# Performance work log

Measured on AMD Instinct MI355X. Metric: run time of the kernel, lower is better.

The kernel has to match this reference:

```python
import jax, jax.numpy as jnp
import numpy as np


def segment_softmax(logits, seg, num_seg):
    m = jax.ops.segment_max(logits, seg, num_segments=num_seg)
    z = jnp.exp(logits - m[seg])
    s = jax.ops.segment_sum(z, seg, num_segments=num_seg)
    return z / s[seg]


def hconv(x_lin, edge_node, edge_he, num_nodes, num_edges, bias, alpha=None):
    # PyG HypergraphConv (heads=1, concat=True): D^-1 H W_e B^-1 H^T X Theta
    ones = jnp.ones(edge_node.shape[0], x_lin.dtype)
    D = jax.ops.segment_sum(ones, edge_node, num_segments=num_nodes)
    Dinv = jnp.where(D > 0, 1.0 / D, 0.0)
    Bd = jax.ops.segment_sum(ones, edge_he, num_segments=num_edges)
    Binv = jnp.where(Bd > 0, 1.0 / Bd, 0.0)
    # node -> hyperedge
    msg = Binv[edge_he][:, None] * x_lin[edge_node]
    if alpha is not None:
        msg = alpha[:, None] * msg
    e = jax.ops.segment_sum(msg, edge_he, num_segments=num_edges)
    # hyperedge -> node
    msg2 = Dinv[edge_node][:, None] * e[edge_he]
    if alpha is not None:
        msg2 = alpha[:, None] * msg2
    out = jax.ops.segment_sum(msg2, edge_node, num_segments=num_nodes)
    return out + bias


def reference(c_it, medicine_it, c_embeddings, m_embeddings, W_conv, b_conv, W_gat, att, b_gat, he_attr):
    nd = c_embeddings.shape[0]  # all indicators are 1 -> nonzero indexing is identity
    nm = m_embeddings.shape[0]
    oc = W_conv.shape[0]

    # diagnosis hypergraph: single hyperedge containing all diseases
    dia_x = c_embeddings @ W_conv.T  # [nd, oc]
    dia_nf = hconv(dia_x, jnp.arange(nd), jnp.zeros(nd, jnp.int32), nd, 1, b_conv)

    # medicine hypergraph: single hyperedge containing all medicines
    med_x = m_embeddings @ W_conv.T  # [nm, oc]
    med_nf = hconv(med_x, jnp.arange(nm), jnp.zeros(nm, jnp.int32), nm, 1, b_conv)

    # dia-med hypergraph: nd hyperedges, hyperedge d = {disease d} U {all medicines}
    comb = jnp.concatenate([c_embeddings, m_embeddings], axis=0)  # [nd+nm, in]
    x_lin = comb @ W_gat.T                                        # [nd+nm, oc]
    he_lin = he_attr @ W_gat.T                                    # [nd, oc]
    med_nodes = jnp.arange(nd, nd + nm)
    edge_node = jnp.concatenate(
        [jnp.arange(nd)[:, None], jnp.broadcast_to(med_nodes[None, :], (nd, nm))], axis=1
    ).reshape(-1)                              # [nd*(nm+1)]
    edge_he = jnp.repeat(jnp.arange(nd), nm + 1)

    # attention (attention_mode='node'): alpha from source node + hyperedge attr, softmax per hyperedge
    a_node = x_lin @ att[:oc]   # [nd+nm]
    a_he = he_lin @ att[oc:]    # [nd]
    logits = jax.nn.leaky_relu(a_node[edge_node] + a_he[edge_he], 0.2)
    alpha = segment_softmax(logits, edge_he, nd)

    dm_nf = hconv(x_lin, edge_node, edge_he, nd + nm, nd, b_gat, alpha)  # [nd+nm, oc]

    disease_final = jnp.concatenate([dm_nf[:nd], dia_nf], axis=1)   # [nd, 2*oc]
    medicine_final = jnp.concatenate([dm_nf[nd:], med_nf], axis=1)  # [nm, 2*oc]
    return jnp.concatenate([disease_final, medicine_final], axis=0)  # [nd+nm, 2*oc]


def setup_inputs() -> dict:
    key = jax.random.key(0)
    ks = jax.random.split(key, 8)
    ND, NM, IN, OUT = 2048, 512, 256, 128
    s = 0.05
    return {
        "c_it": jnp.ones((ND,), jnp.int32),
        "medicine_it": jnp.ones((NM,), jnp.int32),
        "c_embeddings": jax.random.normal(ks[0], (ND, IN), jnp.float32),
        "m_embeddings": jax.random.normal(ks[1], (NM, IN), jnp.float32),
        "W_conv": jax.random.normal(ks[2], (OUT, IN), jnp.float32) * s,
        "b_conv": jax.random.normal(ks[3], (OUT,), jnp.float32) * s,
        "W_gat": jax.random.normal(ks[4], (OUT, IN), jnp.float32) * s,
        "att": jax.random.normal(ks[5], (2 * OUT,), jnp.float32) * s,
        "b_gat": jax.random.normal(ks[6], (OUT,), jnp.float32) * s,
        "he_attr": jax.random.normal(ks[7], (ND, IN), jnp.float32),
    }
```

## Files before the change

kernel.cpp:

```cpp
#include <hip/hip_runtime.h>

#define ND 2048
#define NM 512
#define DIN 256
#define OC 128
#define NTOT (ND + NM)
#define NE (NM + 1)

#define WS_MEANC 0
#define WS_MEANM 256
#define WS_WE    512
#define WS_DIA   768
#define WS_MED   896
#define WS_AHE   1024
#define WS_ANODE 3072
#define WS_CD    5632
#define WS_XLIN  7680
#define WS_PART1 (WS_XLIN + NTOT * OC)
#define WS_PART2 (WS_PART1 + 84 * 256)

__device__ __forceinline__ float lrelu(float x) { return x > 0.f ? x : 0.2f * x; }

__global__ void kA1(const float* __restrict__ c_emb, const float* __restrict__ m_emb,
                    const float* __restrict__ W_gat, const float* __restrict__ att,
                    float* __restrict__ ws) {
    const int b = blockIdx.x;
    const int t = threadIdx.x;
    float acc = 0.f;
    if (b < 64) {
        const float* src = c_emb + (size_t)b * 32 * DIN;
        for (int r = 0; r < 32; ++r) acc += src[r * DIN + t];
    } else if (b < 80) {
        const float* src = m_emb + (size_t)(b - 64) * 32 * DIN;
        for (int r = 0; r < 32; ++r) acc += src[r * DIN + t];
    } else {
        const int o0 = (b - 80) * 32;
        for (int r = 0; r < 32; ++r)
            acc += W_gat[(size_t)(o0 + r) * DIN + t] * att[OC + o0 + r];
    }
    ws[WS_PART1 + b * 256 + t] = acc;
}

__global__ void kA2(float* __restrict__ ws) {
    const int t = threadIdx.x;
    const float* p = ws + WS_PART1;
    float sc = 0.f, sm = 0.f, sw = 0.f;
    for (int b = 0;  b < 64; ++b) sc += p[b * 256 + t];
    for (int b = 64; b < 80; ++b) sm += p[b * 256 + t];
    for (int b = 80; b < 84; ++b) sw += p[b * 256 + t];
    ws[WS_MEANC + t] = sc * (1.f / ND);
    ws[WS_MEANM + t] = sm * (1.f / NM);
    ws[WS_WE + t]    = sw;
}

__global__ void kB(const float* __restrict__ W_conv, const float* __restrict__ b_conv,
                   const float* __restrict__ he_attr, float* __restrict__ ws) {
    if (blockIdx.x == 0) {
        const int o = threadIdx.x;
        if (o < OC) {
            const float* mc = ws + WS_MEANC;
            const float* mm = ws + WS_MEANM;
            const float* wr = W_conv + (size_t)o * DIN;
            float a = 0.f, b = 0.f;
            for (int i = 0; i < DIN; ++i) {
                float w = wr[i];
                a = fmaf(mc[i], w, a);
                b = fmaf(mm[i], w, b);
            }
            float bc = b_conv[o];
            ws[WS_DIA + o] = a + bc;
            ws[WS_MED + o] = b + bc;
        }
    } else {
        const int d = blockIdx.x - 1;
        const int t = threadIdx.x;
        float p = he_attr[(size_t)d * DIN + t] * ws[WS_WE + t];
        for (int m = 1; m < 64; m <<= 1) p += __shfl_xor(p, m, 64);
        __shared__ float s[4];
        if ((t & 63) == 0) s[t >> 6] = p;
        __syncthreads();
        if (t == 0) ws[WS_AHE + d] = s[0] + s[1] + s[2] + s[3];
    }
}

__global__ void kC(const float* __restrict__ c_emb, const float* __restrict__ m_emb,
                   const float* __restrict__ W_gat, const float* __restrict__ att,
                   float* __restrict__ ws) {
    const int d0 = blockIdx.x * 4;
    const int t = threadIdx.x;
    __shared__ float row[4][DIN];
    for (int r = 0; r < 4; ++r) {
        const int d = d0 + r;
        const float* src = (d < ND) ? (c_emb + (size_t)d * DIN)
                                    : (m_emb + (size_t)(d - ND) * DIN);
        float2 u = ((const float2*)src)[t];
        row[r][2 * t] = u.x;
        row[r][2 * t + 1] = u.y;
    }
    __syncthreads();
    const float4* wr = (const float4*)(W_gat + (size_t)t * DIN);
    float a0 = 0.f, a1 = 0.f, a2 = 0.f, a3 = 0.f;
#pragma unroll 8
    for (int v = 0; v < DIN / 4; ++v) {
        float4 w = wr[v];
        const int ib = v * 4;
        a0 = fmaf(row[0][ib], w.x, a0); a0 = fmaf(row[0][ib+1], w.y, a0);
        a0 = fmaf(row[0][ib+2], w.z, a0); a0 = fmaf(row[0][ib+3], w.w, a0);
        a1 = fmaf(row[1][ib], w.x, a1); a1 = fmaf(row[1][ib+1], w.y, a1);
        a1 = fmaf(row[1][ib+2], w.z, a1); a1 = fmaf(row[1][ib+3], w.w, a1);
        a2 = fmaf(row[2][ib], w.x, a2); a2 = fmaf(row[2][ib+1], w.y, a2);
        a2 = fmaf(row[2][ib+2], w.z, a2); a2 = fmaf(row[2][ib+3], w.w, a2);
        a3 = fmaf(row[3][ib], w.x, a3); a3 = fmaf(row[3][ib+1], w.y, a3);
        a3 = fmaf(row[3][ib+2], w.z, a3); a3 = fmaf(row[3][ib+3], w.w, a3);
    }
    float* xl = ws + WS_XLIN + (size_t)d0 * OC;
    xl[0 * OC + t] = a0; xl[1 * OC + t] = a1; xl[2 * OC + t] = a2; xl[3 * OC + t] = a3;
    const float at = att[t];
    __shared__ float s[4][OC];
    s[0][t] = a0 * at; s[1][t] = a1 * at; s[2][t] = a2 * at; s[3][t] = a3 * at;
    __syncthreads();
    for (int st = 64; st > 0; st >>= 1) {
        if (t < st) {
#pragma unroll
            for (int r = 0; r < 4; ++r) s[r][t] += s[r][t + st];
        }
        __syncthreads();
    }
    if (t < 4) ws[WS_ANODE + d0 + t] = s[t][0];
}

#define DT 8
__global__ void kD(const float* __restrict__ b_gat, float* __restrict__ ws,
                   float* __restrict__ out) {
    const int d0 = blockIdx.x * DT;
    const int t = threadIdx.x;
    const int r = t >> 5, l = t & 31;
    __shared__ float zbuf[DT][NE];
    __shared__ float anm[NM];
    __shared__ float ec[DT][OC];
    __shared__ float sinv[DT];
    const float* a_node = ws + WS_ANODE;
    anm[t] = a_node[ND + t];
    anm[t + 256] = a_node[ND + t + 256];
    __syncthreads();
    {
        const int d = d0 + r;
        const float ahe = ws[WS_AHE + d];
        float lmax = -3.4e38f;
        for (int j = l; j < NE; j += 32) {
            float v = (j == 0) ? a_node[d] : anm[j - 1];
            float lg = lrelu(v + ahe);
            zbuf[r][j] = lg;
            lmax = fmaxf(lmax, lg);
        }
        for (int m = 1; m < 32; m <<= 1) lmax = fmaxf(lmax, __shfl_xor(lmax, m, 32));
        float ssum = 0.f;
        for (int j = l; j < NE; j += 32) {
            float z = __expf(zbuf[r][j] - lmax);
            zbuf[r][j] = z;
            ssum += z;
        }
        for (int m = 1; m < 32; m <<= 1) ssum += __shfl_xor(ssum, m, 32);
        if (l == 0) {
            sinv[r] = 1.f / ssum;
            ws[WS_CD + d] = lmax + __logf(ssum);
        }
    }
    __syncthreads();
    const int o = t & (OC - 1);
    const int h = t >> 7;
    float acc[DT];
#pragma unroll
    for (int k = 0; k < DT; ++k) acc[k] = 0.f;
    const float* xm = ws + WS_XLIN + (size_t)ND * OC;
#pragma unroll 4
    for (int j = h * 256; j < h * 256 + 256; ++j) {
        float xv = xm[(size_t)j * OC + o];
#pragma unroll
        for (int k = 0; k < DT; ++k) acc[k] = fmaf(zbuf[k][j + 1], xv, acc[k]);
    }
    if (h == 1) {
#pragma unroll
        for (int k = 0; k < DT; ++k) ec[k][o] = acc[k];
    }
    __syncthreads();
    if (h == 0) {
        const float bg = b_gat[o];
        const float dv = ws[WS_DIA + o];
#pragma unroll
        for (int k = 0; k < DT; ++k) {
            const int d = d0 + k;
            const float inv = sinv[k];
            const float z0 = zbuf[k][0];
            const float xown = ws[WS_XLIN + (size_t)d * OC + o];
            float ev = fmaf(z0, xown, acc[k] + ec[k][o]) * inv * (1.f / NE);
            ws[WS_XLIN + (size_t)d * OC + o] = ev;
            out[(size_t)d * 2 * OC + o]      = fmaf(z0 * inv, ev, bg);
            out[(size_t)d * 2 * OC + OC + o] = dv;
        }
    }
}

__global__ void kE1(float* __restrict__ ws) {
    const int g = blockIdx.x, c = blockIdx.y;
    const int t = threadIdx.x;
    __shared__ float zb[256][16];
    const float* a_node = ws + WS_ANODE;
    const float* ahe = ws + WS_AHE;
    const float* C = ws + WS_CD;
    for (int idx = t; idx < 4096; idx += 256) {
        const int mi = idx & 15, dd = idx >> 4;
        const int d = c * 256 + dd;
        zb[dd][mi] = __expf(lrelu(a_node[ND + g * 16 + mi] + ahe[d]) - C[d]);
    }
    __syncthreads();
    const int o = t & (OC - 1);
    const int h = t >> 7;
    float acc[16];
#pragma unroll
    for (int k = 0; k < 16; ++k) acc[k] = 0.f;
    const float* e = ws + WS_XLIN;
#pragma unroll 2
    for (int dd = h * 128; dd < h * 128 + 128; ++dd) {
        float ev = e[(size_t)(c * 256 + dd) * OC + o];
#pragma unroll
        for (int k = 0; k < 16; ++k) acc[k] = fmaf(zb[dd][k], ev, acc[k]);
    }
    __shared__ float ec[16][OC];
    if (h == 1) {
#pragma unroll
        for (int k = 0; k < 16; ++k) ec[k][o] = acc[k];
    }
    __syncthreads();
    if (h == 0) {
        float* part = ws + WS_PART2 + (size_t)(g * 8 + c) * 16 * OC;
#pragma unroll
        for (int k = 0; k < 16; ++k) part[k * OC + o] = acc[k] + ec[k][o];
    }
}

__global__ void kE2(const float* __restrict__ b_gat, const float* __restrict__ ws,
                    float* __restrict__ out) {
    const int m = blockIdx.x;
    const int o = threadIdx.x;
    const int g = m >> 4, k = m & 15;
    const float* part = ws + WS_PART2;
    float s = 0.f;
#pragma unroll
    for (int c = 0; c < 8; ++c) s += part[((size_t)(g * 8 + c) * 16 + k) * OC + o];
    out[(size_t)(ND + m) * 2 * OC + o]      = fmaf(s, 1.f / ND, b_gat[o]);
    out[(size_t)(ND + m) * 2 * OC + OC + o] = ws[WS_MED + o];
}

extern "C" void kernel_launch(void* const* d_in, const int* in_sizes, int n_in,
                              void* d_out, int out_size, void* d_ws, size_t ws_size,
                              hipStream_t stream) {
    const float* c_emb   = (const float*)d_in[2];
    const float* m_emb   = (const float*)d_in[3];
    const float* W_conv  = (const float*)d_in[4];
    const float* b_conv  = (const float*)d_in[5];
    const float* W_gat   = (const float*)d_in[6];
    const float* att     = (const float*)d_in[7];
    const float* b_gat   = (const float*)d_in[8];
    const float* he_attr = (const float*)d_in[9];
    float* ws  = (float*)d_ws;
    float* out = (float*)d_out;

    hipLaunchKernelGGL(kA1, dim3(84),        dim3(256), 0, stream, c_emb, m_emb, W_gat, att, ws);
    hipLaunchKernelGGL(kA2, dim3(1),         dim3(256), 0, stream, ws);
    hipLaunchKernelGGL(kC,  dim3(NTOT / 4),  dim3(128), 0, stream, c_emb, m_emb, W_gat, att, ws);
    hipLaunchKernelGGL(kB,  dim3(ND + 1),    dim3(256), 0, stream, W_conv, b_conv, he_attr, ws);
    hipLaunchKernelGGL(kD,  dim3(ND / DT),   dim3(256), 0, stream, b_gat, ws, out);
    hipLaunchKernelGGL(kE1, dim3(32, 8),     dim3(256), 0, stream, ws);
    hipLaunchKernelGGL(kE2, dim3(NM),        dim3(128), 0, stream, b_gat, ws, out);
}
```

Baseline: 152.6 us.

## Fuse all seven kernels into one cooperative persistent kernel with grid syncs

```diff
diff --git a/kernel.cpp b/kernel.cpp
--- a/kernel.cpp
+++ b/kernel.cpp
@@ -1,11 +1,15 @@
 #include <hip/hip_runtime.h>
+#include <hip/hip_cooperative_groups.h>
+
+namespace cg = cooperative_groups;
 
 #define ND 2048
 #define NM 512
 #define DIN 256
 #define OC 128
-#define NTOT (ND + NM)
-#define NE (NM + 1)
+#define NTOT 2560
+#define NE 513
+#define NB 256
 
 #define WS_MEANC 0
 #define WS_MEANM 256
@@ -15,241 +19,234 @@
 #define WS_AHE   1024
 #define WS_ANODE 3072
 #define WS_CD    5632
-#define WS_XLIN  7680
-#define WS_PART1 (WS_XLIN + NTOT * OC)
-#define WS_PART2 (WS_PART1 + 84 * 256)
+#define WS_PARTC 7680
+#define WS_PARTM (WS_PARTC + 256*256)
+#define WS_PARTW (WS_PARTM + 256*256)
+#define WS_XLIN  (WS_PARTW + 128*256)
+#define WS_PART2 (WS_XLIN + NTOT*OC)
 
 __device__ __forceinline__ float lrelu(float x) { return x > 0.f ? x : 0.2f * x; }
 
-__global__ void kA1(const float* __restrict__ c_emb, const float* __restrict__ m_emb,
-                    const float* __restrict__ W_gat, const float* __restrict__ att,
-                    float* __restrict__ ws) {
-    const int b = blockIdx.x;
-    const int t = threadIdx.x;
-    float acc = 0.f;
-    if (b < 64) {
-        const float* src = c_emb + (size_t)b * 32 * DIN;
-        for (int r = 0; r < 32; ++r) acc += src[r * DIN + t];
-    } else if (b < 80) {
-        const float* src = m_emb + (size_t)(b - 64) * 32 * DIN;
-        for (int r = 0; r < 32; ++r) acc += src[r * DIN + t];
-    } else {
-        const int o0 = (b - 80) * 32;
-        for (int r = 0; r < 32; ++r)
-            acc += W_gat[(size_t)(o0 + r) * DIN + t] * att[OC + o0 + r];
-    }
-    ws[WS_PART1 + b * 256 + t] = acc;
-}
-
-__global__ void kA2(float* __restrict__ ws) {
-    const int t = threadIdx.x;
-    const float* p = ws + WS_PART1;
-    float sc = 0.f, sm = 0.f, sw = 0.f;
-    for (int b = 0;  b < 64; ++b) sc += p[b * 256 + t];
-    for (int b = 64; b < 80; ++b) sm += p[b * 256 + t];
-    for (int b = 80; b < 84; ++b) sw += p[b * 256 + t];
-    ws[WS_MEANC + t] = sc * (1.f / ND);
-    ws[WS_MEANM + t] = sm * (1.f / NM);
-    ws[WS_WE + t]    = sw;
-}
-
-__global__ void kB(const float* __restrict__ W_conv, const float* __restrict__ b_conv,
-                   const float* __restrict__ he_attr, float* __restrict__ ws) {
-    if (blockIdx.x == 0) {
-        const int o = threadIdx.x;
-        if (o < OC) {
-            const float* mc = ws + WS_MEANC;
-            const float* mm = ws + WS_MEANM;
-            const float* wr = W_conv + (size_t)o * DIN;
-            float a = 0.f, b = 0.f;
+__global__ void __launch_bounds__(256, 1) kFused(
+        const float* __restrict__ c_emb, const float* __restrict__ m_emb,
+        const float* __restrict__ W_conv, const float* __restrict__ b_conv,
+        const float* __restrict__ W_gat, const float* __restrict__ att,
+        const float* __restrict__ b_gat, const float* __restrict__ he_attr,
+        float* __restrict__ ws, float* __restrict__ out) {
+    cg::grid_group grid = cg::this_grid();
+    __shared__ float smem[6400];
+    const int b = blockIdx.x, t = threadIdx.x;
+
+    {
+        float sc = 0.f;
+        const float* srcc = c_emb + (size_t)b * 8 * DIN;
+#pragma unroll
+        for (int r = 0; r < 8; ++r) sc += srcc[r * DIN + t];
+        ws[WS_PARTC + b * 256 + t] = sc;
+        ws[WS_PARTM + b * 256 + t] = m_emb[(size_t)(2 * b) * DIN + t]
+                                   + m_emb[(size_t)(2 * b + 1) * DIN + t];
+        if (b < OC) ws[WS_PARTW + b * 256 + t] = W_gat[(size_t)b * DIN + t] * att[OC + b];
+
+        float (*row)[DIN] = (float(*)[DIN])smem;
+        float (*sA)[OC]   = (float(*)[OC])(smem + 10 * DIN);
+        const int d0 = b * 10;
+#pragma unroll
+        for (int p = 0; p < 5; ++p) {
+            const int r = 2 * p + (t >> 7);
+            const int d = d0 + r;
+            const float* src = (d < ND) ? c_emb + (size_t)d * DIN
+                                        : m_emb + (size_t)(d - ND) * DIN;
+            float2 u = ((const float2*)src)[t & 127];
+            row[r][2 * (t & 127)]     = u.x;
+            row[r][2 * (t & 127) + 1] = u.y;
+        }
+        __syncthreads();
+        const int o = t & (OC - 1), h = t >> 7;
+        float acc[5] = {0.f, 0.f, 0.f, 0.f, 0.f};
+        const float4* wr = (const float4*)(W_gat + (size_t)o * DIN);
+        for (int v = 0; v < 64; ++v) {
+            const float4 w = wr[v];
+            const int ib = 4 * v;
+#pragma unroll
+            for (int k = 0; k < 5; ++k) {
+                const float* rw = row[5 * h + k] + ib;
+                acc[k] = fmaf(rw[0], w.x, acc[k]);
+                acc[k] = fmaf(rw[1], w.y, acc[k]);
+                acc[k] = fmaf(rw[2], w.z, acc[k]);
+                acc[k] = fmaf(rw[3], w.w, acc[k]);
+            }
+        }
+        const float at = att[o];
+#pragma unroll
+        for (int k = 0; k < 5; ++k) {
+            ws[WS_XLIN + (size_t)(d0 + 5 * h + k) * OC + o] = acc[k];
+            sA[5 * h + k][o] = acc[k] * at;
+        }
+        __syncthreads();
+#pragma unroll
+        for (int st = 64; st >= 1; st >>= 1) {
+            for (int idx = t; idx < 10 * st; idx += 256) {
+                const int r = idx / st, i = idx - r * st;
+                sA[r][i] += sA[r][i + st];
+            }
+            __syncthreads();
+        }
+        if (t < 10) ws[WS_ANODE + d0 + t] = sA[t][0];
+    }
+    grid.sync();
+
+    if (b == 0) {
+        float sc = 0.f, sm = 0.f, sw = 0.f;
+        for (int bb = 0; bb < 256; ++bb) sc += ws[WS_PARTC + bb * 256 + t];
+        for (int bb = 0; bb < 256; ++bb) sm += ws[WS_PARTM + bb * 256 + t];
+        for (int bb = 0; bb < 128; ++bb) sw += ws[WS_PARTW + bb * 256 + t];
+        ws[WS_MEANC + t] = sc * (1.f / ND);
+        ws[WS_MEANM + t] = sm * (1.f / NM);
+        ws[WS_WE + t]    = sw;
+        __syncthreads();
+        if (t < OC) {
+            const float* wrr = W_conv + (size_t)t * DIN;
+            float a = 0.f, m2 = 0.f;
             for (int i = 0; i < DIN; ++i) {
-                float w = wr[i];
-                a = fmaf(mc[i], w, a);
-                b = fmaf(mm[i], w, b);
-            }
-            float bc = b_conv[o];
-            ws[WS_DIA + o] = a + bc;
-            ws[WS_MED + o] = b + bc;
-        }
-    } else {
-        const int d = blockIdx.x - 1;
-        const int t = threadIdx.x;
-        float p = he_attr[(size_t)d * DIN + t] * ws[WS_WE + t];
-        for (int m = 1; m < 64; m <<= 1) p += __shfl_xor(p, m, 64);
-        __shared__ float s[4];
-        if ((t & 63) == 0) s[t >> 6] = p;
-        __syncthreads();
-        if (t == 0) ws[WS_AHE + d] = s[0] + s[1] + s[2] + s[3];
-    }
-}
-
-__global__ void kC(const float* __restrict__ c_emb, const float* __restrict__ m_emb,
-                   const float* __restrict__ W_gat, const float* __restrict__ att,
-                   float* __restrict__ ws) {
-    const int d0 = blockIdx.x * 4;
-    const int t = threadIdx.x;
-    __shared__ float row[4][DIN];
-    for (int r = 0; r < 4; ++r) {
-        const int d = d0 + r;
-        const float* src = (d < ND) ? (c_emb + (size_t)d * DIN)
-                                    : (m_emb + (size_t)(d - ND) * DIN);
-        float2 u = ((const float2*)src)[t];
-        row[r][2 * t] = u.x;
-        row[r][2 * t + 1] = u.y;
-    }
-    __syncthreads();
-    const float4* wr = (const float4*)(W_gat + (size_t)t * DIN);
-    float a0 = 0.f, a1 = 0.f, a2 = 0.f, a3 = 0.f;
-#pragma unroll 8
-    for (int v = 0; v < DIN / 4; ++v) {
-        float4 w = wr[v];
-        const int ib = v * 4;
-        a0 = fmaf(row[0][ib], w.x, a0); a0 = fmaf(row[0][ib+1], w.y, a0);
-        a0 = fmaf(row[0][ib+2], w.z, a0); a0 = fmaf(row[0][ib+3], w.w, a0);
-        a1 = fmaf(row[1][ib], w.x, a1); a1 = fmaf(row[1][ib+1], w.y, a1);
-        a1 = fmaf(row[1][ib+2], w.z, a1); a1 = fmaf(row[1][ib+3], w.w, a1);
-        a2 = fmaf(row[2][ib], w.x, a2); a2 = fmaf(row[2][ib+1], w.y, a2);
-        a2 = fmaf(row[2][ib+2], w.z, a2); a2 = fmaf(row[2][ib+3], w.w, a2);
-        a3 = fmaf(row[3][ib], w.x, a3); a3 = fmaf(row[3][ib+1], w.y, a3);
-        a3 = fmaf(row[3][ib+2], w.z, a3); a3 = fmaf(row[3][ib+3], w.w, a3);
-    }
-    float* xl = ws + WS_XLIN + (size_t)d0 * OC;
-    xl[0 * OC + t] = a0; xl[1 * OC + t] = a1; xl[2 * OC + t] = a2; xl[3 * OC + t] = a3;
-    const float at = att[t];
-    __shared__ float s[4][OC];
-    s[0][t] = a0 * at; s[1][t] = a1 * at; s[2][t] = a2 * at; s[3][t] = a3 * at;
-    __syncthreads();
-    for (int st = 64; st > 0; st >>= 1) {
-        if (t < st) {
-#pragma unroll
-            for (int r = 0; r < 4; ++r) s[r][t] += s[r][t + st];
-        }
-        __syncthreads();
-    }
-    if (t < 4) ws[WS_ANODE + d0 + t] = s[t][0];
-}
-
-#define DT 8
-__global__ void kD(const float* __restrict__ b_gat, float* __restrict__ ws,
-                   float* __restrict__ out) {
-    const int d0 = blockIdx.x * DT;
-    const int t = threadIdx.x;
-    const int r = t >> 5, l = t & 31;
-    __shared__ float zbuf[DT][NE];
-    __shared__ float anm[NM];
-    __shared__ float ec[DT][OC];
-    __shared__ float sinv[DT];
-    const float* a_node = ws + WS_ANODE;
-    anm[t] = a_node[ND + t];
-    anm[t + 256] = a_node[ND + t + 256];
-    __syncthreads();
-    {
-        const int d = d0 + r;
-        const float ahe = ws[WS_AHE + d];
+                const float w = wrr[i];
+                a  = fmaf(ws[WS_MEANC + i], w, a);
+                m2 = fmaf(ws[WS_MEANM + i], w, m2);
+            }
+            const float bc = b_conv[t];
+            ws[WS_DIA + t] = a + bc;
+            ws[WS_MED + t] = m2 + bc;
+        }
+    }
+    grid.sync();
+
+    {
+        float (*zbuf)[8] = (float(*)[8])smem;
+        float* anm  = smem + 4112;
+        float (*ec)[OC] = (float(*)[OC])(smem + 4112 + 512);
+        float* sinv = smem + 4112 + 512 + 8 * OC;
+        anm[t]       = ws[WS_ANODE + ND + t];
+        anm[t + 256] = ws[WS_ANODE + ND + 256 + t];
+        __syncthreads();
+        const int r = t >> 5, l = t & 31;
+        const int d = b * 8 + r;
+        const float* he = he_attr + (size_t)d * DIN;
+        float ah = 0.f;
+        for (int i = l; i < DIN; i += 32) ah = fmaf(he[i], ws[WS_WE + i], ah);
+#pragma unroll
+        for (int m = 1; m < 32; m <<= 1) ah += __shfl_xor(ah, m, 32);
+        if (l == 0) ws[WS_AHE + d] = ah;
+        const float an_d = ws[WS_ANODE + d];
         float lmax = -3.4e38f;
         for (int j = l; j < NE; j += 32) {
-            float v = (j == 0) ? a_node[d] : anm[j - 1];
-            float lg = lrelu(v + ahe);
-            zbuf[r][j] = lg;
+            const float v = (j == 0) ? an_d : anm[j - 1];
+            const float lg = lrelu(v + ah);
+            zbuf[j][r] = lg;
             lmax = fmaxf(lmax, lg);
         }
+#pragma unroll
         for (int m = 1; m < 32; m <<= 1) lmax = fmaxf(lmax, __shfl_xor(lmax, m, 32));
-        float ssum = 0.f;
+        float ss = 0.f;
         for (int j = l; j < NE; j += 32) {
-            float z = __expf(zbuf[r][j] - lmax);
-            zbuf[r][j] = z;
-            ssum += z;
-        }
-        for (int m = 1; m < 32; m <<= 1) ssum += __shfl_xor(ssum, m, 32);
-        if (l == 0) {
-            sinv[r] = 1.f / ssum;
-            ws[WS_CD + d] = lmax + __logf(ssum);
-        }
-    }
-    __syncthreads();
-    const int o = t & (OC - 1);
-    const int h = t >> 7;
-    float acc[DT];
-#pragma unroll
-    for (int k = 0; k < DT; ++k) acc[k] = 0.f;
-    const float* xm = ws + WS_XLIN + (size_t)ND * OC;
-#pragma unroll 4
-    for (int j = h * 256; j < h * 256 + 256; ++j) {
-        float xv = xm[(size_t)j * OC + o];
-#pragma unroll
-        for (int k = 0; k < DT; ++k) acc[k] = fmaf(zbuf[k][j + 1], xv, acc[k]);
-    }
-    if (h == 1) {
-#pragma unroll
-        for (int k = 0; k < DT; ++k) ec[k][o] = acc[k];
-    }
-    __syncthreads();
-    if (h == 0) {
-        const float bg = b_gat[o];
-        const float dv = ws[WS_DIA + o];
-#pragma unroll
-        for (int k = 0; k < DT; ++k) {
-            const int d = d0 + k;
-            const float inv = sinv[k];
-            const float z0 = zbuf[k][0];
-            const float xown = ws[WS_XLIN + (size_t)d * OC + o];
-            float ev = fmaf(z0, xown, acc[k] + ec[k][o]) * inv * (1.f / NE);
-            ws[WS_XLIN + (size_t)d * OC + o] = ev;
-            out[(size_t)d * 2 * OC + o]      = fmaf(z0 * inv, ev, bg);
-            out[(size_t)d * 2 * OC + OC + o] = dv;
-        }
-    }
-}
-
-__global__ void kE1(float* __restrict__ ws) {
-    const int g = blockIdx.x, c = blockIdx.y;
-    const int t = threadIdx.x;
-    __shared__ float zb[256][16];
-    const float* a_node = ws + WS_ANODE;
-    const float* ahe = ws + WS_AHE;
-    const float* C = ws + WS_CD;
-    for (int idx = t; idx < 4096; idx += 256) {
-        const int mi = idx & 15, dd = idx >> 4;
-        const int d = c * 256 + dd;
-        zb[dd][mi] = __expf(lrelu(a_node[ND + g * 16 + mi] + ahe[d]) - C[d]);
-    }
-    __syncthreads();
-    const int o = t & (OC - 1);
-    const int h = t >> 7;
-    float acc[16];
-#pragma unroll
-    for (int k = 0; k < 16; ++k) acc[k] = 0.f;
-    const float* e = ws + WS_XLIN;
-#pragma unroll 2
-    for (int dd = h * 128; dd < h * 128 + 128; ++dd) {
-        float ev = e[(size_t)(c * 256 + dd) * OC + o];
-#pragma unroll
-        for (int k = 0; k < 16; ++k) acc[k] = fmaf(zb[dd][k], ev, acc[k]);
-    }
-    __shared__ float ec[16][OC];
-    if (h == 1) {
-#pragma unroll
-        for (int k = 0; k < 16; ++k) ec[k][o] = acc[k];
-    }
-    __syncthreads();
-    if (h == 0) {
-        float* part = ws + WS_PART2 + (size_t)(g * 8 + c) * 16 * OC;
-#pragma unroll
-        for (int k = 0; k < 16; ++k) part[k * OC + o] = acc[k] + ec[k][o];
-    }
-}
-
-__global__ void kE2(const float* __restrict__ b_gat, const float* __restrict__ ws,
-                    float* __restrict__ out) {
-    const int m = blockIdx.x;
-    const int o = threadIdx.x;
-    const int g = m >> 4, k = m & 15;
-    const float* part = ws + WS_PART2;
-    float s = 0.f;
-#pragma unroll
-    for (int c = 0; c < 8; ++c) s += part[((size_t)(g * 8 + c) * 16 + k) * OC + o];
-    out[(size_t)(ND + m) * 2 * OC + o]      = fmaf(s, 1.f / ND, b_gat[o]);
-    out[(size_t)(ND + m) * 2 * OC + OC + o] = ws[WS_MED + o];
+            const float z = __expf(zbuf[j][r] - lmax);
+            zbuf[j][r] = z;
+            ss += z;
+        }
+#pragma unroll
+        for (int m = 1; m < 32; m <<= 1) ss += __shfl_xor(ss, m, 32);
+        if (l == 0) { sinv[r] = 1.f / ss; ws[WS_CD + d] = lmax + __logf(ss); }
+        __syncthreads();
+        const int o = t & (OC - 1), h = t >> 7;
+        float acc[8] = {0, 0, 0, 0, 0, 0, 0, 0};
+        const float* xm = ws + WS_XLIN + (size_t)ND * OC;
+        for (int j = h * 256; j < h * 256 + 256; ++j) {
+            const float xv = xm[(size_t)j * OC + o];
+            const float4* zr = (const float4*)zbuf[j + 1];
+            const float4 za = zr[0], zb4 = zr[1];
+            acc[0] = fmaf(za.x,  xv, acc[0]);
+            acc[1] = fmaf(za.y,  xv, acc[1]);
+            acc[2] = fmaf(za.z,  xv, acc[2]);
+            acc[3] = fmaf(za.w,  xv, acc[3]);
+            acc[4] = fmaf(zb4.x, xv, acc[4]);
+            acc[5] = fmaf(zb4.y, xv, acc[5]);
+            acc[6] = fmaf(zb4.z, xv, acc[6]);
+            acc[7] = fmaf(zb4.w, xv, acc[7]);
+        }
+        if (h == 1) {
+#pragma unroll
+            for (int k = 0; k < 8; ++k) ec[k][o] = acc[k];
+        }
+        __syncthreads();
+        if (h == 0) {
+            const float bg = b_gat[o];
+            const float dv = ws[WS_DIA + o];
+#pragma unroll
+            for (int k = 0; k < 8; ++k) {
+                const int dd = b * 8 + k;
+                const float inv = sinv[k];
+                const float z0 = zbuf[0][k];
+                const float xown = ws[WS_XLIN + (size_t)dd * OC + o];
+                const float ev = fmaf(z0, xown, acc[k] + ec[k][o]) * inv * (1.f / NE);
+                ws[WS_XLIN + (size_t)dd * OC + o] = ev;
+                out[(size_t)dd * 2 * OC + o]      = fmaf(z0 * inv, ev, bg);
+                out[(size_t)dd * 2 * OC + OC + o] = dv;
+            }
+        }
+    }
+    grid.sync();
+
+    {
+        const int g = b >> 3, c = b & 7;
+        float (*zb)[16]  = (float(*)[16])smem;
+        float (*ec2)[OC] = (float(*)[OC])(smem + 4096);
+        for (int idx = t; idx < 4096; idx += 256) {
+            const int mi = idx & 15, dd = idx >> 4;
+            const int d = c * 256 + dd;
+            zb[dd][mi] = __expf(lrelu(ws[WS_ANODE + ND + g * 16 + mi] + ws[WS_AHE + d])
+                                - ws[WS_CD + d]);
+        }
+        __syncthreads();
+        const int o = t & (OC - 1), h = t >> 7;
+        float acc[16];
+#pragma unroll
+        for (int k = 0; k < 16; ++k) acc[k] = 0.f;
+        const float* e = ws + WS_XLIN;
+        for (int dd = h * 128; dd < h * 128 + 128; ++dd) {
+            const float ev = e[(size_t)(c * 256 + dd) * OC + o];
+            const float4* zr = (const float4*)zb[dd];
+            const float4 z0 = zr[0], z1 = zr[1], z2 = zr[2], z3 = zr[3];
+            acc[0]  = fmaf(z0.x, ev, acc[0]);   acc[1]  = fmaf(z0.y, ev, acc[1]);
+            acc[2]  = fmaf(z0.z, ev, acc[2]);   acc[3]  = fmaf(z0.w, ev, acc[3]);
+            acc[4]  = fmaf(z1.x, ev, acc[4]);   acc[5]  = fmaf(z1.y, ev, acc[5]);
+            acc[6]  = fmaf(z1.z, ev, acc[6]);   acc[7]  = fmaf(z1.w, ev, acc[7]);
+            acc[8]  = fmaf(z2.x, ev, acc[8]);   acc[9]  = fmaf(z2.y, ev, acc[9]);
+            acc[10] = fmaf(z2.z, ev, acc[10]);  acc[11] = fmaf(z2.w, ev, acc[11]);
+            acc[12] = fmaf(z3.x, ev, acc[12]);  acc[13] = fmaf(z3.y, ev, acc[13]);
+            acc[14] = fmaf(z3.z, ev, acc[14]);  acc[15] = fmaf(z3.w, ev, acc[15]);
+        }
+        if (h == 1) {
+#pragma unroll
+            for (int k = 0; k < 16; ++k) ec2[k][o] = acc[k];
+        }
+        __syncthreads();
+        if (h == 0) {
+            float* part = ws + WS_PART2 + (size_t)(g * 8 + c) * 16 * OC;
+#pragma unroll
+            for (int k = 0; k < 16; ++k) part[k * OC + o] = acc[k] + ec2[k][o];
+        }
+    }
+    grid.sync();
+
+    {
+        const int o = t & (OC - 1);
+        const int m = 2 * b + (t >> 7);
+        const int g = m >> 4, k = m & 15;
+        float s = 0.f;
+#pragma unroll
+        for (int c = 0; c < 8; ++c)
+            s += ws[WS_PART2 + ((size_t)(g * 8 + c) * 16 + k) * OC + o];
+        out[(size_t)(ND + m) * 2 * OC + o]      = fmaf(s, 1.f / ND, b_gat[o]);
+        out[(size_t)(ND + m) * 2 * OC + OC + o] = ws[WS_MED + o];
+    }
 }
 
 extern "C" void kernel_launch(void* const* d_in, const int* in_sizes, int n_in,
@@ -266,11 +263,8 @@
     float* ws  = (float*)d_ws;
     float* out = (float*)d_out;
 
-    hipLaunchKernelGGL(kA1, dim3(84),        dim3(256), 0, stream, c_emb, m_emb, W_gat, att, ws);
-    hipLaunchKernelGGL(kA2, dim3(1),         dim3(256), 0, stream, ws);
-    hipLaunchKernelGGL(kC,  dim3(NTOT / 4),  dim3(128), 0, stream, c_emb, m_emb, W_gat, att, ws);
-    hipLaunchKernelGGL(kB,  dim3(ND + 1),    dim3(256), 0, stream, W_conv, b_conv, he_attr, ws);
-    hipLaunchKernelGGL(kD,  dim3(ND / DT),   dim3(256), 0, stream, b_gat, ws, out);
-    hipLaunchKernelGGL(kE1, dim3(32, 8),     dim3(256), 0, stream, ws);
-    hipLaunchKernelGGL(kE2, dim3(NM),        dim3(128), 0, stream, b_gat, ws, out);
+    void* args[] = { &c_emb, &m_emb, &W_conv, &b_conv, &W_gat,
+                     &att, &b_gat, &he_attr, &ws, &out };
+    hipLaunchCooperativeKernel((const void*)kFused, dim3(NB), dim3(256),
+                               args, 0, stream);
 }
```

After: 289.3 us. +89.5%, slower.
